# Kernel optimization log

Measured on AMD Instinct MI355X. Metric: run time of the kernel, lower is better.

The kernel has to match this reference:

```python
import math
import jax, jax.numpy as jnp
import numpy as np

E_EDGES = 65536
N_NODES = 8192
MUL = 32
LAT = 128
COND = 32
# uuu tensor-product instructions (l1, l2, l_out) generated by the selection-rule loop
INSTR = [(0,0,0),(1,1,0),(2,2,0),
         (0,1,1),(1,0,1),(1,1,1),(1,2,1),(2,1,1),(2,2,1),
         (0,2,2),(1,1,2),(1,2,2),(2,0,2),(2,1,2),(2,2,2)]

# ---- real Wigner-3j (invariant 3-tensor) via null space of equivariance constraints ----
def _su2_J(l):
    m = np.arange(-l, l + 1)
    Jz = np.diag(m).astype(complex)
    d = 2 * l + 1
    Jp = np.zeros((d, d), complex)
    Jp[np.arange(1, d), np.arange(0, d - 1)] = np.sqrt((l - m[:-1]) * (l + m[:-1] + 1))
    Jm = Jp.conj().T
    return (Jp + Jm) / 2, (Jp - Jm) / 2j, Jz

def _q(l):
    q = np.zeros((2 * l + 1, 2 * l + 1), complex)
    for m in range(-l, 0):
        q[l + m, l + abs(m)] = 1 / np.sqrt(2)
        q[l + m, l - abs(m)] = -1j / np.sqrt(2)
    q[l, l] = 1.0
    for m in range(1, l + 1):
        q[l + m, l + abs(m)] = (-1) ** m / np.sqrt(2)
        q[l + m, l - abs(m)] = 1j * (-1) ** m / np.sqrt(2)
    return q

def _gen(l):
    q = _q(l)
    return [np.real(q.conj().T @ (-1j * J) @ q) for J in _su2_J(l)]

def _w3j(l1, l2, l3):
    G1, G2, G3 = _gen(l1), _gen(l2), _gen(l3)
    d1, d2, d3 = 2 * l1 + 1, 2 * l2 + 1, 2 * l3 + 1
    rows = []
    for a in range(3):
        rows.append(np.kron(np.kron(G1[a], np.eye(d2)), np.eye(d3))
                    + np.kron(np.kron(np.eye(d1), G2[a]), np.eye(d3))
                    + np.kron(np.kron(np.eye(d1), np.eye(d2)), G3[a]))
    _, _, vt = np.linalg.svd(np.concatenate(rows, 0))
    c = vt[-1]
    c = c / np.linalg.norm(c)
    c = c * np.sign(c[np.argmax(np.abs(c))])
    return c.reshape(d1, d2, d3).astype(np.float32)

W3J = {}
for _k in INSTR:
    if _k not in W3J:
        W3J[_k] = jnp.asarray(_w3j(*_k))

def _split9(x):
    # (E, MUL, 9) -> per-l blocks (widths 1,3,5)
    return (x[:, :, 0:1], x[:, :, 1:4], x[:, :, 4:9])

def _so3_ln(blocks, gamma, eps=1e-6):
    out = []
    for b, x in enumerate(blocks):
        if x.shape[-1] == 1:  # scalars: centered layernorm over channels
            mu = jnp.mean(x, axis=1, keepdims=True)
            var = jnp.mean((x - mu) ** 2, axis=1, keepdims=True)
            x = (x - mu) * jax.lax.rsqrt(var + eps)
        else:  # l>0: RMS over (channel, m), no centering (equivariance)
            ms = jnp.mean(x ** 2, axis=(1, 2), keepdims=True)
            x = x * jax.lax.rsqrt(ms + eps)
        out.append(x * gamma[b][None, :, None])
    return out

def _forward(scalar_latent, equiv_latent, edge_conditioning, update_coeff,
             W_env, b_env0, gamma_env, Wg_env, bg_env, gamma_tp,
             W1_s, b1_s, W2_s, b2_s, Weq0, beq0, Weq1, Weq2, Wg_eq, bg_eq,
             edge_index, active_edges):
    E = scalar_latent.shape[0]
    edge_center = edge_index[0]
    # env_eq: per-l SO3 linear (channel mixing), bias on l=0
    xb = _split9(equiv_latent)
    env = [jnp.einsum('eum,vu->evm', xb[l], W_env[l]) for l in range(3)]
    env[0] = env[0] + b_env0[None, :, None]
    gate_in = jnp.concatenate([scalar_latent, edge_conditioning], axis=-1)  # (E,160)
    g_env = 1.0 + 0.1 * jnp.tanh(gate_in @ Wg_env + bg_env[0])
    env_edges = jnp.concatenate(env, axis=-1) * g_env[:, None, None]
    # scatter-sum edges -> nodes, SO3 layernorm, gather back per edge
    env_nodes = jax.ops.segment_sum(env_edges, edge_center, num_segments=N_NODES)
    env_nodes = jnp.concatenate(_so3_ln(_split9(env_nodes), gamma_env), axis=-1)
    local = env_nodes[edge_center]  # (E, MUL, 9)
    # selection-rule-sparse tensor product, uuu, component-normalized
    x1b = _split9(equiv_latent)
    x2b = _split9(local)
    tp_blocks = [math.sqrt(2 * lo + 1) * jnp.einsum('ijk,eui,euj->euk', W3J[(l1, l2, lo)], x1b[l1], x2b[l2])
                 for (l1, l2, lo) in INSTR]
    tp_blocks = _so3_ln(tp_blocks, gamma_tp)
    # scalar (l=0) slices -> (E, 3*MUL)
    tp_scalars = jnp.concatenate(tp_blocks[0:3], axis=-1).reshape(E, -1)
    scalar_in = jnp.concatenate([tp_scalars, edge_conditioning], axis=-1)
    new_scalar = jax.nn.silu(scalar_in @ W1_s.T + b1_s) @ W2_s.T + b2_s  # (E, LAT)
    # equiv_update: SO3 linear tp_out_irreps -> equiv_latent_irreps
    x0 = tp_scalars  # (E, 3*MUL)
    out0 = (x0 @ Weq0.T + beq0)[:, :, None]                      # (E, MUL, 1)
    out1 = jnp.einsum('eum,vu->evm', jnp.concatenate(tp_blocks[3:9], axis=1), Weq1)   # (E, MUL, 3)
    out2 = jnp.einsum('eum,vu->evm', jnp.concatenate(tp_blocks[9:15], axis=1), Weq2)  # (E, MUL, 5)
    new_equiv = jnp.concatenate([out0, out1, out2], axis=-1)
    g_eq = 1.0 + 0.1 * jnp.tanh(gate_in @ Wg_eq + bg_eq[0])
    new_equiv = new_equiv * g_eq[:, None, None]
    # residual stream with update coefficient + index_add over active_edges
    c = update_coeff[0]
    co = jax.lax.rsqrt(c * c + 1.0)
    cn = c * co
    s_out = (co * scalar_latent).at[active_edges].add(cn * new_scalar)
    e_out = (co * equiv_latent).at[active_edges].add(cn * new_equiv)
    return s_out, e_out

def setup_inputs() -> dict:
    key = jax.random.key(0)
    ks = jax.random.split(key, 16)
    f32 = jnp.float32
    return {
        'scalar_latent': jax.random.normal(ks[0], (E_EDGES, LAT), f32),
        'equiv_latent': jax.random.normal(ks[1], (E_EDGES, MUL, 9), f32),
        'edge_conditioning': jax.random.normal(ks[2], (E_EDGES, COND), f32),
        'update_coeff': jnp.ones((1,), f32),
        'W_env': jax.random.normal(ks[3], (3, MUL, MUL), f32) / math.sqrt(MUL),
        'b_env0': jnp.zeros((MUL,), f32),
        'gamma_env': jnp.ones((3, MUL), f32),
        'Wg_env': jax.random.normal(ks[4], (LAT + COND,), f32) / math.sqrt(LAT + COND),
        'bg_env': jnp.zeros((1,), f32),
        'gamma_tp': jnp.ones((15, MUL), f32),
        'W1_s': jax.random.normal(ks[5], (LAT, 3 * MUL + COND), f32) / math.sqrt(3 * MUL + COND),
        'b1_s': jnp.zeros((LAT,), f32),
        'W2_s': jax.random.normal(ks[6], (LAT, LAT), f32) / math.sqrt(LAT),
        'b2_s': jnp.zeros((LAT,), f32),
        'Weq0': jax.random.normal(ks[7], (MUL, 3 * MUL), f32) / math.sqrt(3 * MUL),
        'beq0': jnp.zeros((MUL,), f32),
        'Weq1': jax.random.normal(ks[8], (MUL, 6 * MUL), f32) / math.sqrt(6 * MUL),
        'Weq2': jax.random.normal(ks[9], (MUL, 6 * MUL), f32) / math.sqrt(6 * MUL),
        'Wg_eq': jax.random.normal(ks[10], (LAT + COND,), f32) / math.sqrt(LAT + COND),
        'bg_eq': jnp.zeros((1,), f32),
        'edge_index': jax.random.randint(ks[11], (2, E_EDGES), 0, N_NODES),
        'active_edges': jnp.arange(E_EDGES),
    }

def reference(scalar_latent, equiv_latent, edge_conditioning, update_coeff,
              W_env, b_env0, gamma_env, Wg_env, bg_env, gamma_tp,
              W1_s, b1_s, W2_s, b2_s, Weq0, beq0, Weq1, Weq2, Wg_eq, bg_eq,
              edge_index, active_edges):
    return _forward(scalar_latent, equiv_latent, edge_conditioning, update_coeff,
                    W_env, b_env0, gamma_env, Wg_env, bg_env, gamma_tp,
                    W1_s, b1_s, W2_s, b2_s, Weq0, beq0, Weq1, Weq2, Wg_eq, bg_eq,
                    edge_index, active_edges)
```

## Files before the change

kernel.cpp:

```cpp
#include <hip/hip_runtime.h>
#include <math.h>

#define E_EDGES 65536
#define N_NODES 8192

typedef _Float16 half_t;
typedef _Float16 h8 __attribute__((ext_vector_type(8)));
typedef float f4 __attribute__((ext_vector_type(4)));

#define SSC_P 136

#define C3f   0.57735026918962576f
#define C5f   0.44721359549995794f
#define C10f  0.31622776601683794f
#define C30f  0.18257418583505536f
#define C30x2 0.36514837167011072f
#define A235  0.23904572186687872f
#define B370  0.20701966780270626f
#define C70f  0.11952286093343936f
#define S3f   1.7320508075688772f
#define S5f   2.2360679774997896f
#define S5n  -2.2360679774997896f


__device__ double factd(int n) { double r = 1.0; for (int i = 2; i <= n; ++i) r *= i; return r; }

__device__ double w3j_m(int j1, int j2, int j3, int m1, int m2, int m3) {
  if (m1 + m2 + m3 != 0) return 0.0;
  if (abs(m1) > j1 || abs(m2) > j2 || abs(m3) > j3) return 0.0;
  double delta = sqrt(factd(j1 + j2 - j3) * factd(j1 - j2 + j3) * factd(-j1 + j2 + j3)
                      / factd(j1 + j2 + j3 + 1));
  double pref = sqrt(factd(j1 + m1) * factd(j1 - m1) * factd(j2 + m2) * factd(j2 - m2)
                     * factd(j3 + m3) * factd(j3 - m3));
  int klo = max(0, max(j2 - j3 - m1, j1 + m2 - j3));
  int khi = min(j1 + j2 - j3, min(j1 - m1, j2 + m2));
  double s = 0.0;
  for (int k = klo; k <= khi; ++k) {
    double d = factd(k) * factd(j1 + j2 - j3 - k) * factd(j1 - m1 - k) * factd(j2 + m2 - k)
             * factd(j3 - j2 + m1 + k) * factd(j3 - j1 - m2 + k);
    s += ((k & 1) ? -1.0 : 1.0) / d;
  }
  int e = j1 - j2 - m3;
  double sg = ((e % 2 + 2) % 2) ? -1.0 : 1.0;
  return sg * delta * pref * s;
}

__device__ void qent(int l, int mr, int col, double* re, double* im) {
  const double v = 0.7071067811865475244;
  *re = 0.0; *im = 0.0;
  int m = mr - l;
  if (m < 0) {
    if (col == l - m) *re = v;
    else if (col == l + m) *im = -v;
  } else if (m == 0) {
    if (col == l) *re = 1.0;
  } else {
    double s = (m & 1) ? -1.0 : 1.0;
    if (col == l + m) *re = s * v;
    else if (col == l - m) *im = s * v;
  }
}

__constant__ const int GB_L1[15] = {0,1,2,0,1,1,1,2,2,0,1,1,2,2,2};
__constant__ const int GB_L2[15] = {0,1,2,1,0,1,2,1,2,2,1,2,0,1,2};
__constant__ const int GB_LO[15] = {0,0,0,1,1,1,1,1,1,2,2,2,2,2,2};
__constant__ const int GB_WOFF[15] = {0,1,10,35,44,53,80,125,170,245,270,315,390,415,490};
__constant__ const double GB_FLIP[15] = {1,1,1,1,1,-1,1,1,1,1,1,1,1,-1,-1};

extern "C" __global__ __launch_bounds__(128)
void gen_w3j(float* __restrict__ w3j_out) {
  __shared__ double vsh[128];
  __shared__ double red[128];
  __shared__ int redi[128];
  const int b = blockIdx.x;
  const int t = threadIdx.x;
  const int l1 = GB_L1[b], l2 = GB_L2[b], l3 = GB_LO[b];
  const int d1 = 2 * l1 + 1, d2 = 2 * l2 + 1, d3 = 2 * l3 + 1;
  const int n = d1 * d2 * d3;
  double tre = 0.0, tim = 0.0;
  if (t < n) {
    int a = t / (d2 * d3), r = t - a * (d2 * d3), bb = r / d3, c = r - bb * d3;
    for (int mr1 = 0; mr1 < d1; ++mr1) {
      double q1r, q1i; qent(l1, mr1, a, &q1r, &q1i); q1i = -q1i;
      if (q1r == 0.0 && q1i == 0.0) continue;
      int m1 = mr1 - l1;
      for (int mr2 = 0; mr2 < d2; ++mr2) {
        double q2r, q2i; qent(l2, mr2, bb, &q2r, &q2i); q2i = -q2i;
        if (q2r == 0.0 && q2i == 0.0) continue;
        int m2 = mr2 - l2;
        int m3 = -(m1 + m2);
        if (m3 < -l3 || m3 > l3) continue;
        double q3r, q3i; qent(l3, m3 + l3, c, &q3r, &q3i); q3i = -q3i;
        if (q3r == 0.0 && q3i == 0.0) continue;
        double w = w3j_m(l1, l2, l3, m1, m2, m3);
        if (w == 0.0) continue;
        double ar = q1r * q2r - q1i * q2i, ai = q1r * q2i + q1i * q2r;
        double cr = ar * q3r - ai * q3i, ci = ar * q3i + ai * q3r;
        tre += cr * w; tim += ci * w;
      }
    }
  }
  red[t] = tre * tre; __syncthreads();
  for (int s = 64; s; s >>= 1) { if (t < s) red[t] += red[t + s]; __syncthreads(); }
  double nre = red[0]; __syncthreads();
  red[t] = tim * tim; __syncthreads();
  for (int s = 64; s; s >>= 1) { if (t < s) red[t] += red[t + s]; __syncthreads(); }
  double nim = red[0]; __syncthreads();
  double v = (nre >= nim) ? tre : tim;
  v *= 1.0 / sqrt(nre >= nim ? nre : nim);
  red[t] = fabs(v); __syncthreads();
  for (int s = 64; s; s >>= 1) { if (t < s) red[t] = fmax(red[t], red[t + s]); __syncthreads(); }
  double mx = red[0]; __syncthreads();
  redi[t] = (t < n && fabs(v) >= mx * (1.0 - 1e-6)) ? t : 1 << 20; __syncthreads();
  for (int s = 64; s; s >>= 1) { if (t < s) redi[t] = min(redi[t], redi[t + s]); __syncthreads(); }
  int win = redi[0];
  vsh[t] = v; __syncthreads();
  double sgn = (vsh[win] < 0.0) ? -1.0 : 1.0;
  const double norm3[3] = {1.0, 1.7320508075688772, 2.2360679774997896};
  if (t < n) w3j_out[GB_WOFF[b] + t] = (float)(v * sgn * GB_FLIP[b] * norm3[l3]);
}

extern "C" __global__ __launch_bounds__(256)
void prep_weights(const float* __restrict__ W1, const float* __restrict__ W2,
                  const float* __restrict__ Weq0, const float* __restrict__ Weq1,
                  const float* __restrict__ Weq2,
                  half_t* __restrict__ W1F, half_t* __restrict__ W2F,
                  half_t* __restrict__ Weq0F, half_t* __restrict__ Weq1F,
                  half_t* __restrict__ Weq2F) {
  int t = blockIdx.x * blockDim.x + threadIdx.x;
  int stride = gridDim.x * blockDim.x;
  for (int f = t; f < 16384; f += stride) {
    int i = f & 7, lane = (f >> 3) & 63, ks = (f >> 9) & 3, nt = f >> 11;
    int n = nt * 16 + (lane & 15);
    int k = ks * 32 + (lane >> 4) * 8 + i;
    W1F[f] = (half_t)W1[n * 128 + k];
    W2F[f] = (half_t)W2[n * 128 + k];
  }
  for (int f = t; f < 3072; f += stride) {
    int i = f & 7, lane = (f >> 3) & 63, rest = f >> 9;
    int ks = rest % 3, nt = rest / 3;
    int n = nt * 16 + (lane & 15);
    int k = ks * 32 + (lane >> 4) * 8 + i;
    Weq0F[f] = (half_t)Weq0[n * 96 + k];
  }
  for (int f = t; f < 6144; f += stride) {
    int i = f & 7, lane = (f >> 3) & 63, rest = f >> 9;
    int ks = rest % 6, nt = rest / 6;
    int n = nt * 16 + (lane & 15);
    int k = ks * 32 + (lane >> 4) * 8 + i;
    Weq1F[f] = (half_t)Weq1[n * 192 + k];
    Weq2F[f] = (half_t)Weq2[n * 192 + k];
  }
}

extern "C" __global__ __launch_bounds__(256)
void gate_count(const float* __restrict__ scalar, const float* __restrict__ cond,
                const float* __restrict__ Wg_env, const float* __restrict__ bg_env,
                const float* __restrict__ Wg_eq, const float* __restrict__ bg_eq,
                const int* __restrict__ edge_index,
                float* __restrict__ g_env, float* __restrict__ g_eq,
                int* __restrict__ counts) {
  const int t = threadIdx.x;
  const int e0 = blockIdx.x * 8;
  const int eg = t >> 5, lane = t & 31;
  size_t e = (size_t)(e0 + eg);
  float pa = 0.f, pb = 0.f;
  for (int i = lane; i < 160; i += 32) {
    float xi = (i < 128) ? scalar[e * 128 + i] : cond[e * 32 + (i - 128)];
    pa = fmaf(xi, Wg_env[i], pa);
    pb = fmaf(xi, Wg_eq[i], pb);
  }
  for (int off = 16; off; off >>= 1) { pa += __shfl_xor(pa, off); pb += __shfl_xor(pb, off); }
  if (lane == 0) {
    g_env[e] = 1.f + 0.1f * tanhf(pa + bg_env[0]);
    g_eq[e]  = 1.f + 0.1f * tanhf(pb + bg_eq[0]);
  }
  if (t < 8) atomicAdd(&counts[edge_index[e0 + t]], 1);
}

extern "C" __global__ __launch_bounds__(256)
void csr_scan(int* __restrict__ counts, int* __restrict__ offsets) {
  __shared__ int part[256];
  __shared__ int pre[257];
  const int t = threadIdx.x;
  const int base = t * 32;
  int s = 0;
  for (int i = 0; i < 32; ++i) s += counts[base + i];
  part[t] = s; __syncthreads();
  if (t == 0) { int a = 0; for (int i = 0; i < 256; ++i) { pre[i] = a; a += part[i]; } pre[256] = a; }
  __syncthreads();
  int run = pre[t];
  for (int i = 0; i < 32; ++i) {
    int c = counts[base + i];
    offsets[base + i] = run;
    counts[base + i] = run;
    run += c;
  }
  if (t == 0) offsets[N_NODES] = pre[256];
}

extern "C" __global__ __launch_bounds__(256)
void csr_fill(const int* __restrict__ edge_index, int* __restrict__ cursor,
              int* __restrict__ elist) {
  int e = blockIdx.x * 256 + threadIdx.x;
  if (e < E_EDGES) {
    int pos = atomicAdd(&cursor[edge_index[e]], 1);
    elist[pos] = e;
  }
}

extern "C" __global__ __launch_bounds__(128)
void env_build(const float* __restrict__ equiv, const float* __restrict__ g_env,
               const int* __restrict__ elist, const int* __restrict__ offsets,
               const float* __restrict__ W_env, const float* __restrict__ b_env0,
               const float* __restrict__ gamma_env, float* __restrict__ env_nodes) {
  __shared__ float xs[288];
  const int n = blockIdx.x, t = threadIdx.x;
  const int lo = offsets[n], hi = offsets[n + 1];
  float acc0 = 0.f, acc1 = 0.f, acc2 = 0.f, gsum = 0.f;
  for (int idx = lo; idx < hi; ++idx) {
    int e = elist[idx];
    float g = g_env[e];
    gsum += g;
    const float* row = equiv + (size_t)e * 288;
    acc0 = fmaf(g, row[t], acc0);
    acc1 = fmaf(g, row[t + 128], acc1);
    if (t < 32) acc2 = fmaf(g, row[t + 256], acc2);
  }
  xs[t] = acc0; xs[t + 128] = acc1;
  if (t < 32) xs[t + 256] = acc2;
  __syncthreads();
  float ev[9];
  if (t < 32) {
    const int v = t;
#pragma unroll
    for (int m = 0; m < 9; ++m) {
      int l = (m == 0) ? 0 : (m < 4 ? 1 : 2);
      const float4* Wr = (const float4*)(W_env + (size_t)(l * 32 + v) * 32);
      float s = 0.f;
#pragma unroll
      for (int u4 = 0; u4 < 8; ++u4) {
        float4 wv = Wr[u4];
        int ub = u4 * 4;
        s = fmaf(wv.x, xs[(ub + 0) * 9 + m], s);
        s = fmaf(wv.y, xs[(ub + 1) * 9 + m], s);
        s = fmaf(wv.z, xs[(ub + 2) * 9 + m], s);
        s = fmaf(wv.w, xs[(ub + 3) * 9 + m], s);
      }
      if (m == 0) s += b_env0[v] * gsum;
      ev[m] = s;
    }
    float s0 = ev[0], q0 = ev[0] * ev[0];
#pragma unroll
    for (int off = 16; off; off >>= 1) { s0 += __shfl_xor(s0, off); q0 += __shfl_xor(q0, off); }
    float mean0 = s0 * (1.f / 32.f);
    float var0 = q0 * (1.f / 32.f) - mean0 * mean0;
    float r0 = rsqrtf(var0 + 1e-6f);
    float q1 = ev[1] * ev[1] + ev[2] * ev[2] + ev[3] * ev[3];
#pragma unroll
    for (int off = 16; off; off >>= 1) q1 += __shfl_xor(q1, off);
    float r1 = rsqrtf(q1 * (1.f / 96.f) + 1e-6f);
    float q2 = ev[4]*ev[4] + ev[5]*ev[5] + ev[6]*ev[6] + ev[7]*ev[7] + ev[8]*ev[8];
#pragma unroll
    for (int off = 16; off; off >>= 1) q2 += __shfl_xor(q2, off);
    float r2 = rsqrtf(q2 * (1.f / 160.f) + 1e-6f);
    ev[0] = (ev[0] - mean0) * r0 * gamma_env[v];
    float g1 = r1 * gamma_env[32 + v], g2 = r2 * gamma_env[64 + v];
    ev[1] *= g1; ev[2] *= g1; ev[3] *= g1;
    ev[4] *= g2; ev[5] *= g2; ev[6] *= g2; ev[7] *= g2; ev[8] *= g2;
  }
  __syncthreads();
  if (t < 32) {
#pragma unroll
    for (int m = 0; m < 9; ++m) xs[t * 9 + m] = ev[m];
  }
  __syncthreads();
  float* outb = env_nodes + (size_t)n * 288;
  outb[t] = xs[t]; outb[t + 128] = xs[t + 128];
  if (t < 32) outb[t + 256] = xs[t + 256];
}

extern "C" __global__ __launch_bounds__(512, 4)
void edge_update(const float* __restrict__ scalar, const float* __restrict__ equiv,
                 const float* __restrict__ cond, const float* __restrict__ updc,
                 const float* __restrict__ env_nodes, const float* __restrict__ gamma_tp,
                 const half_t* __restrict__ W1F, const float* __restrict__ b1,
                 const half_t* __restrict__ W2F, const float* __restrict__ b2,
                 const half_t* __restrict__ Weq0F, const float* __restrict__ beq0,
                 const half_t* __restrict__ Weq1F, const half_t* __restrict__ Weq2F,
                 const float* __restrict__ g_eq,
                 const int* __restrict__ edge_index, const int* __restrict__ active_edges,
                 const float* __restrict__ w3j, float* __restrict__ out_s,
                 float* __restrict__ out_e) {
  __shared__ __align__(16) half_t stp[48 * 16 * 32];
  __shared__ __align__(16) half_t ssc[16 * SSC_P];
  __shared__ __align__(16) half_t shh[16 * SSC_P];
  __shared__ float sg[16];
  __shared__ int snode[16];
  __shared__ int sact[16];
  const int t = threadIdx.x;
  const int e0 = blockIdx.x * 16;
  const float cc = updc[0];
  const float co = rsqrtf(cc * cc + 1.f);
  const float cn = cc * co;

  if (t < 16) {
    snode[t] = edge_index[e0 + t];
    sact[t] = active_edges[e0 + t];
    sg[t] = g_eq[e0 + t];
  }
  {
    int e = t >> 5, j = t & 31;
    ssc[e * SSC_P + 96 + j] = (half_t)cond[(size_t)(e0 + e) * 32 + j];
  }
  __syncthreads();

  {
    const int eg = t >> 5, u = t & 31;
    const float* arow = equiv + (size_t)(e0 + eg) * 288 + u * 9;
    const float* brow = env_nodes + (size_t)snode[eg] * 288 + u * 9;
    float a0 = arow[0], b0 = brow[0];
    float A1[3] = {arow[1], arow[2], arow[3]};
    float A2[5] = {arow[4], arow[5], arow[6], arow[7], arow[8]};
    float B1[3] = {brow[1], brow[2], brow[3]};
    float B2[5] = {brow[4], brow[5], brow[6], brow[7], brow[8]};
    float o[51];
    o[0] = a0 * b0;
    o[1] = C3f * (A1[0]*B1[0] + A1[1]*B1[1] + A1[2]*B1[2]);
    o[2] = C5f * (A2[0]*B2[0] + A2[1]*B2[1] + A2[2]*B2[2] + A2[3]*B2[3] + A2[4]*B2[4]);
    o[3] = a0 * B1[0]; o[4] = a0 * B1[1]; o[5] = a0 * B1[2];
    o[6] = A1[0] * b0; o[7] = A1[1] * b0; o[8] = A1[2] * b0;
    o[9] = o[10] = o[11] = 0.f;
#pragma unroll
    for (int i = 0; i < 3; ++i)
#pragma unroll
      for (int j = 0; j < 3; ++j) {
        float p = A1[i] * B1[j];
#pragma unroll
        for (int k = 0; k < 3; ++k)
          o[9 + k] = fmaf(w3j[53 + (i * 3 + j) * 3 + k], p, o[9 + k]);
      }
    o[12] = S3f * (C10f*(A1[1]*B2[1] + A1[2]*B2[0]) - C30f*A1[0]*B2[2] - C10f*A1[0]*B2[4]);
    o[13] = S3f * (C10f*(A1[0]*B2[1] + A1[2]*B2[3]) + C30x2*A1[1]*B2[2]);
    o[14] = S3f * (C10f*(A1[0]*B2[0] + A1[1]*B2[3] + A1[2]*B2[4]) - C30f*A1[2]*B2[2]);
    o[15] = S3f * (C10f*(A2[1]*B1[1] + A2[0]*B1[2]) - C30f*A2[2]*B1[0] - C10f*A2[4]*B1[0]);
    o[16] = S3f * (C10f*(A2[1]*B1[0] + A2[3]*B1[2]) + C30x2*A2[2]*B1[1]);
    o[17] = S3f * (C10f*(A2[0]*B1[0] + A2[3]*B1[1] + A2[4]*B1[2]) - C30f*A2[2]*B1[2]);
    o[18] = o[19] = o[20] = 0.f;
#pragma unroll
    for (int i = 0; i < 5; ++i)
#pragma unroll
      for (int j = 0; j < 5; ++j) {
        float p = A2[i] * B2[j];
#pragma unroll
        for (int k = 0; k < 3; ++k)
          o[18 + k] = fmaf(w3j[170 + (i * 5 + j) * 3 + k], p, o[18 + k]);
      }
    o[21] = a0 * B2[0]; o[22] = a0 * B2[1]; o[23] = a0 * B2[2]; o[24] = a0 * B2[3]; o[25] = a0 * B2[4];
    o[26] = S5f * C10f * (A1[2]*B1[0] + A1[0]*B1[2]);
    o[27] = S5f * C10f * (A1[0]*B1[1] + A1[1]*B1[0]);
    o[28] = S5f * (C30x2*A1[1]*B1[1] - C30f*(A1[0]*B1[0] + A1[2]*B1[2]));
    o[29] = S5f * C10f * (A1[1]*B1[2] + A1[2]*B1[1]);
    o[30] = S5f * C10f * (A1[2]*B1[2] - A1[0]*B1[0]);
    o[31] = S5f * (C30f*(A1[2]*B2[3] - A1[0]*B2[1]) - C30x2*A1[1]*B2[4]);
    o[32] = S5f * (C30f*(A1[0]*B2[0] - A1[1]*B2[3] + A1[2]*B2[4]) + C10f*A1[2]*B2[2]);
    o[33] = S5f * C10f * (A1[0]*B2[3] - A1[2]*B2[1]);
    o[34] = S5f * (C30f*(A1[1]*B2[1] - A1[2]*B2[0] + A1[0]*B2[4]) - C10f*A1[0]*B2[2]);
    o[35] = S5f * (C30x2*A1[1]*B2[0] - C30f*(A1[2]*B2[1] + A1[0]*B2[3]));
    o[36] = A2[0] * b0; o[37] = A2[1] * b0; o[38] = A2[2] * b0; o[39] = A2[3] * b0; o[40] = A2[4] * b0;
    o[41] = S5n * (C30f*(A2[3]*B1[2] - A2[1]*B1[0]) - C30x2*A2[4]*B1[1]);
    o[42] = S5n * (C30f*(A2[0]*B1[0] - A2[3]*B1[1] + A2[4]*B1[2]) + C10f*A2[2]*B1[2]);
    o[43] = S5n * C10f * (A2[3]*B1[0] - A2[1]*B1[2]);
    o[44] = S5n * (C30f*(A2[1]*B1[1] - A2[0]*B1[2] + A2[4]*B1[0]) - C10f*A2[2]*B1[0]);
    o[45] = S5n * (C30x2*A2[0]*B1[1] - C30f*(A2[1]*B1[2] + A2[3]*B1[0]));
    o[46] = S5n * (A235*(A2[0]*B2[2] + A2[2]*B2[0]) - B370*(A2[1]*B2[3] + A2[3]*B2[1]));
    o[47] = S5n * (-B370*(A2[0]*B2[3] + A2[3]*B2[0]) - C70f*(A2[1]*B2[2] + A2[2]*B2[1]) + B370*(A2[1]*B2[4] + A2[4]*B2[1]));
    o[48] = S5n * (A235*(A2[0]*B2[0] - A2[2]*B2[2] + A2[4]*B2[4]) - C70f*(A2[1]*B2[1] + A2[3]*B2[3]));
    o[49] = S5n * (-B370*(A2[0]*B2[1] + A2[1]*B2[0]) - C70f*(A2[3]*B2[2] + A2[2]*B2[3]) - B370*(A2[3]*B2[4] + A2[4]*B2[3]));
    o[50] = S5n * (B370*(A2[1]*B2[1] - A2[3]*B2[3]) + A235*(A2[2]*B2[4] + A2[4]*B2[2]));

#pragma unroll
    for (int b = 0; b < 3; ++b) {
      float x = o[b];
      float s = x, q = x * x;
#pragma unroll
      for (int off = 16; off; off >>= 1) { s += __shfl_xor(s, off); q += __shfl_xor(q, off); }
      float mean = s * (1.f / 32.f);
      float var = q * (1.f / 32.f) - mean * mean;
      ssc[eg * SSC_P + u * 3 + b] = (half_t)((x - mean) * rsqrtf(var + 1e-6f) * gamma_tp[b * 32 + u]);
    }
    const int offs[12] = {3, 6, 9, 12, 15, 18, 21, 26, 31, 36, 41, 46};
    const int d3s[12]  = {3, 3, 3, 3, 3, 3, 5, 5, 5, 5, 5, 5};
    const int uswz = u ^ ((eg & 3) << 3);
#pragma unroll
    for (int bb = 0; bb < 12; ++bb) {
      float q = 0.f;
#pragma unroll
      for (int k = 0; k < d3s[bb]; ++k) { float x = o[offs[bb] + k]; q += x * x; }
#pragma unroll
      for (int off = 16; off; off >>= 1) q += __shfl_xor(q, off);
      float scale = rsqrtf(q / (32.f * d3s[bb]) + 1e-6f) * gamma_tp[(bb + 3) * 32 + u];
#pragma unroll
      for (int k = 0; k < d3s[bb]; ++k)
        stp[((offs[bb] + k - 3) * 16 + eg) * 32 + uswz] = (half_t)(o[offs[bb] + k] * scale);
    }
  }
  __syncthreads();

  const int l = t & 63, wave = t >> 6;
  const int g = l >> 4, c = l & 15;
  f4 mlp2acc;

  {
    const int nt = wave;
    float bn = b1[nt * 16 + c];
    f4 acc = {bn, bn, bn, bn};
#pragma unroll
    for (int ks = 0; ks < 4; ++ks) {
      h8 a = *(const h8*)&ssc[c * SSC_P + ks * 32 + g * 8];
      h8 b = *(const h8*)&W1F[(((nt * 4 + ks) * 64) + l) * 8];
      acc = __builtin_amdgcn_mfma_f32_16x16x32_f16(a, b, acc, 0, 0, 0);
    }
#pragma unroll
    for (int i = 0; i < 4; ++i) {
      float x = acc[i];
      shh[(4 * g + i) * SSC_P + nt * 16 + c] = (half_t)(x / (1.f + expf(-x)));
    }
  }
  __syncthreads();

  {
    const int nt = wave;
    float bn = b2[nt * 16 + c];
    f4 acc = {bn, bn, bn, bn};
#pragma unroll
    for (int ks = 0; ks < 4; ++ks) {
      h8 a = *(const h8*)&shh[c * SSC_P + ks * 32 + g * 8];
      h8 b = *(const h8*)&W2F[(((nt * 4 + ks) * 64) + l) * 8];
      acc = __builtin_amdgcn_mfma_f32_16x16x32_f16(a, b, acc, 0, 0, 0);
    }
    mlp2acc = acc;
  }

  f4 accT[3];
  int nTiles = 0;
  for (int T = wave; T < 18; T += 8, ++nTiles) {
    f4 acc;
    if (T < 2) {
      const int nt = T;
      float bv = beq0[nt * 16 + c];
      acc = (f4){bv, bv, bv, bv};
#pragma unroll
      for (int ks = 0; ks < 3; ++ks) {
        h8 a = *(const h8*)&ssc[c * SSC_P + ks * 32 + g * 8];
        h8 b = *(const h8*)&Weq0F[(((nt * 3 + ks) * 64) + l) * 8];
        acc = __builtin_amdgcn_mfma_f32_16x16x32_f16(a, b, acc, 0, 0, 0);
      }
    } else if (T < 8) {
      const int idx = T - 2, Mt = idx >> 1, nt = idx & 1;
      const int row = Mt * 16 + c;
      const int e = row / 3, m = row - e * 3;
      const int gx = (g ^ (e & 3)) * 8;
      acc = (f4){0.f, 0.f, 0.f, 0.f};
#pragma unroll
      for (int ks = 0; ks < 6; ++ks) {
        int kk = ks * 3 + m;
        h8 a = *(const h8*)&stp[(kk * 16 + e) * 32 + gx];
        h8 b = *(const h8*)&Weq1F[(((nt * 6 + ks) * 64) + l) * 8];
        acc = __builtin_amdgcn_mfma_f32_16x16x32_f16(a, b, acc, 0, 0, 0);
      }
    } else {
      const int idx = T - 8, Mt = idx >> 1, nt = idx & 1;
      const int row = Mt * 16 + c;
      const int e = row / 5, m = row - e * 5;
      const int gx = (g ^ (e & 3)) * 8;
      acc = (f4){0.f, 0.f, 0.f, 0.f};
#pragma unroll
      for (int ks = 0; ks < 6; ++ks) {
        int kk = 18 + ks * 5 + m;
        h8 a = *(const h8*)&stp[(kk * 16 + e) * 32 + gx];
        h8 b = *(const h8*)&Weq2F[(((nt * 6 + ks) * 64) + l) * 8];
        acc = __builtin_amdgcn_mfma_f32_16x16x32_f16(a, b, acc, 0, 0, 0);
      }
    }
    accT[nTiles] = acc;
  }
  __syncthreads();

  {
    float* tmp  = reinterpret_cast<float*>(&stp[0]);
    float* sout = tmp + 4608;
    int slot = 0;
    for (int T = wave; T < 18; T += 8, ++slot) {
      f4 acc = accT[slot];
      int Mt, nt, type;
      if (T < 2)      { type = 0; Mt = 0; nt = T; }
      else if (T < 8) { type = 1; Mt = (T - 2) >> 1; nt = (T - 2) & 1; }
      else            { type = 2; Mt = (T - 8) >> 1; nt = (T - 8) & 1; }
      const int v = nt * 16 + c;
#pragma unroll
      for (int i = 0; i < 4; ++i) {
        int row = Mt * 16 + 4 * g + i;
        int e, off;
        if (type == 0)      { e = row; off = 0; }
        else if (type == 1) { e = row / 3; off = 1 + (row - e * 3); }
        else                { e = row / 5; off = 4 + (row - e * 5); }
        tmp[e * 288 + v * 9 + off] = cn * sg[e] * acc[i];
      }
    }
    {
      const int nt = wave;
#pragma unroll
      for (int i = 0; i < 4; ++i)
        sout[(4 * g + i) * 128 + nt * 16 + c] = cn * mlp2acc[i];
    }
  }
  __syncthreads();

  {
    const float* tmp  = reinterpret_cast<const float*>(&stp[0]);
    const float* sout = tmp + 4608;
    const float4* tmp4 = (const float4*)tmp;
    for (int i = t; i < 16 * 72; i += 512) {
      int e = i / 72, q = i - e * 72;
      size_t r = (size_t)sact[e];
      const float4 ev = *(const float4*)&equiv[r * 288 + q * 4];
      float4 tv = tmp4[i];
      float4 ov;
      ov.x = co * ev.x + tv.x; ov.y = co * ev.y + tv.y;
      ov.z = co * ev.z + tv.z; ov.w = co * ev.w + tv.w;
      *(float4*)&out_e[r * 288 + q * 4] = ov;
    }
    for (int i = t; i < 16 * 128; i += 512) {
      int e = i >> 7, n = i & 127;
      size_t r = (size_t)sact[e];
      out_s[r * 128 + n] = co * scalar[r * 128 + n] + sout[i];
    }
  }
}

extern "C" void kernel_launch(void* const* d_in, const int* in_sizes, int n_in,
                              void* d_out, int out_size, void* d_ws, size_t ws_size,
                              hipStream_t stream) {
  const float* scalar     = (const float*)d_in[0];
  const float* equiv      = (const float*)d_in[1];
  const float* cond       = (const float*)d_in[2];
  const float* updc       = (const float*)d_in[3];
  const float* W_env      = (const float*)d_in[4];
  const float* b_env0     = (const float*)d_in[5];
  const float* gamma_env  = (const float*)d_in[6];
  const float* Wg_env     = (const float*)d_in[7];
  const float* bg_env     = (const float*)d_in[8];
  const float* gamma_tp   = (const float*)d_in[9];
  const float* W1         = (const float*)d_in[10];
  const float* b1         = (const float*)d_in[11];
  const float* W2         = (const float*)d_in[12];
  const float* b2         = (const float*)d_in[13];
  const float* Weq0       = (const float*)d_in[14];
  const float* beq0       = (const float*)d_in[15];
  const float* Weq1       = (const float*)d_in[16];
  const float* Weq2       = (const float*)d_in[17];
  const float* Wg_eq      = (const float*)d_in[18];
  const float* bg_eq      = (const float*)d_in[19];
  const int* edge_index   = (const int*)d_in[20];
  const int* active_edges = (const int*)d_in[21];

  float* out_s = (float*)d_out;
  float* out_e = out_s + (size_t)E_EDGES * 128;

  float* ws    = (float*)d_ws;
  float* env   = ws;
  float* w3jt  = env + (size_t)N_NODES * 288;
  float* diag  = w3jt + 640;
  half_t* W1F   = (half_t*)(diag + 16);
  half_t* W2F   = W1F + 16384;
  half_t* Weq0F = W2F + 16384;
  half_t* Weq1F = Weq0F + 3072;
  half_t* Weq2F = Weq1F + 6144;
  int* counts  = (int*)(Weq2F + 6144);
  int* offsets = counts + N_NODES;
  float* g_eq  = (float*)(offsets + N_NODES + 1);
  float* g_env = out_s + ((size_t)E_EDGES * (128 + 288) - 131072);
  int* elist   = (int*)(g_env + 65536);

  hipMemsetAsync(counts, 0, N_NODES * sizeof(int), stream);
  gen_w3j<<<15, 128, 0, stream>>>(w3jt);
  prep_weights<<<48, 256, 0, stream>>>(W1, W2, Weq0, Weq1, Weq2,
                                       W1F, W2F, Weq0F, Weq1F, Weq2F);
  gate_count<<<E_EDGES / 8, 256, 0, stream>>>(scalar, cond, Wg_env, bg_env, Wg_eq, bg_eq,
                                              edge_index, g_env, g_eq, counts);
  csr_scan<<<1, 256, 0, stream>>>(counts, offsets);
  csr_fill<<<E_EDGES / 256, 256, 0, stream>>>(edge_index, counts, elist);
  env_build<<<N_NODES, 128, 0, stream>>>(equiv, g_env, elist, offsets,
                                         W_env, b_env0, gamma_env, env);
  edge_update<<<E_EDGES / 16, 512, 0, stream>>>(scalar, equiv, cond, updc, env, gamma_tp,
                                                W1F, b1, W2F, b2, Weq0F, beq0, Weq1F, Weq2F,
                                                g_eq, edge_index, active_edges,
                                                w3jt, out_s, out_e);
}
```

Baseline: 241.6 us.

## Merge gate computation into CSR fill and split env_build gather across two groups

Moves the gate computation out of the counting pass and into the fill pass. The count pass becomes a plain atomic histogram, and the separate fill kernel goes away. env_build now runs 256 threads per node: two groups each accumulate alternating incoming edges, with two edges per iteration for more loads in flight, and the partial sums are combined through shared memory. This targets latency in the per-node gather, at the cost of an extra shared reduction and sync. Edge order within each node's list still depends on atomics.

New measurement: 261.6 us. +8.3%, slower.

```diff
diff --git a/kernel.cpp b/kernel.cpp
--- a/kernel.cpp
+++ b/kernel.cpp
@@ -154,28 +154,9 @@
 }
 
 extern "C" __global__ __launch_bounds__(256)
-void gate_count(const float* __restrict__ scalar, const float* __restrict__ cond,
-                const float* __restrict__ Wg_env, const float* __restrict__ bg_env,
-                const float* __restrict__ Wg_eq, const float* __restrict__ bg_eq,
-                const int* __restrict__ edge_index,
-                float* __restrict__ g_env, float* __restrict__ g_eq,
-                int* __restrict__ counts) {
-  const int t = threadIdx.x;
-  const int e0 = blockIdx.x * 8;
-  const int eg = t >> 5, lane = t & 31;
-  size_t e = (size_t)(e0 + eg);
-  float pa = 0.f, pb = 0.f;
-  for (int i = lane; i < 160; i += 32) {
-    float xi = (i < 128) ? scalar[e * 128 + i] : cond[e * 32 + (i - 128)];
-    pa = fmaf(xi, Wg_env[i], pa);
-    pb = fmaf(xi, Wg_eq[i], pb);
-  }
-  for (int off = 16; off; off >>= 1) { pa += __shfl_xor(pa, off); pb += __shfl_xor(pb, off); }
-  if (lane == 0) {
-    g_env[e] = 1.f + 0.1f * tanhf(pa + bg_env[0]);
-    g_eq[e]  = 1.f + 0.1f * tanhf(pb + bg_eq[0]);
-  }
-  if (t < 8) atomicAdd(&counts[edge_index[e0 + t]], 1);
+void csr_count(const int* __restrict__ edge_index, int* __restrict__ counts) {
+  int e = blockIdx.x * 256 + threadIdx.x;
+  if (e < E_EDGES) atomicAdd(&counts[edge_index[e]], 1);
 }
 
 extern "C" __global__ __launch_bounds__(256)
@@ -200,36 +181,79 @@
 }
 
 extern "C" __global__ __launch_bounds__(256)
-void csr_fill(const int* __restrict__ edge_index, int* __restrict__ cursor,
-              int* __restrict__ elist) {
-  int e = blockIdx.x * 256 + threadIdx.x;
-  if (e < E_EDGES) {
-    int pos = atomicAdd(&cursor[edge_index[e]], 1);
-    elist[pos] = e;
-  }
-}
-
-extern "C" __global__ __launch_bounds__(128)
+void gate_fill(const float* __restrict__ scalar, const float* __restrict__ cond,
+               const float* __restrict__ Wg_env, const float* __restrict__ bg_env,
+               const float* __restrict__ Wg_eq, const float* __restrict__ bg_eq,
+               const int* __restrict__ edge_index,
+               float* __restrict__ g_env, float* __restrict__ g_eq,
+               int* __restrict__ cursor, int* __restrict__ elist) {
+  const int t = threadIdx.x;
+  const int e0 = blockIdx.x * 8;
+  const int eg = t >> 5, lane = t & 31;
+  size_t e = (size_t)(e0 + eg);
+  float pa = 0.f, pb = 0.f;
+  for (int i = lane; i < 160; i += 32) {
+    float xi = (i < 128) ? scalar[e * 128 + i] : cond[e * 32 + (i - 128)];
+    pa = fmaf(xi, Wg_env[i], pa);
+    pb = fmaf(xi, Wg_eq[i], pb);
+  }
+  for (int off = 16; off; off >>= 1) { pa += __shfl_xor(pa, off); pb += __shfl_xor(pb, off); }
+  if (lane == 0) {
+    g_env[e] = 1.f + 0.1f * tanhf(pa + bg_env[0]);
+    g_eq[e]  = 1.f + 0.1f * tanhf(pb + bg_eq[0]);
+  }
+  if (t < 8) {
+    int ge = e0 + t;
+    int pos = atomicAdd(&cursor[edge_index[ge]], 1);
+    elist[pos] = ge;
+  }
+}
+
+extern "C" __global__ __launch_bounds__(256)
 void env_build(const float* __restrict__ equiv, const float* __restrict__ g_env,
                const int* __restrict__ elist, const int* __restrict__ offsets,
                const float* __restrict__ W_env, const float* __restrict__ b_env0,
                const float* __restrict__ gamma_env, float* __restrict__ env_nodes) {
   __shared__ float xs[288];
+  __shared__ float xs2[288];
+  __shared__ float gsums[2];
   const int n = blockIdx.x, t = threadIdx.x;
+  const int grp = t >> 7, tt = t & 127;
   const int lo = offsets[n], hi = offsets[n + 1];
   float acc0 = 0.f, acc1 = 0.f, acc2 = 0.f, gsum = 0.f;
-  for (int idx = lo; idx < hi; ++idx) {
+  int idx = lo + grp;
+  for (; idx + 2 < hi; idx += 4) {
+    int ea = elist[idx], eb = elist[idx + 2];
+    float ga = g_env[ea], gb = g_env[eb];
+    gsum += ga + gb;
+    const float* ra = equiv + (size_t)ea * 288;
+    const float* rb = equiv + (size_t)eb * 288;
+    float a0 = ra[tt], b0 = rb[tt];
+    float a1 = ra[tt + 128], b1v = rb[tt + 128];
+    acc0 = fmaf(ga, a0, acc0); acc0 = fmaf(gb, b0, acc0);
+    acc1 = fmaf(ga, a1, acc1); acc1 = fmaf(gb, b1v, acc1);
+    if (tt < 32) {
+      acc2 = fmaf(ga, ra[tt + 256], acc2);
+      acc2 = fmaf(gb, rb[tt + 256], acc2);
+    }
+  }
+  for (; idx < hi; idx += 2) {
     int e = elist[idx];
     float g = g_env[e];
     gsum += g;
     const float* row = equiv + (size_t)e * 288;
-    acc0 = fmaf(g, row[t], acc0);
-    acc1 = fmaf(g, row[t + 128], acc1);
-    if (t < 32) acc2 = fmaf(g, row[t + 256], acc2);
-  }
-  xs[t] = acc0; xs[t + 128] = acc1;
-  if (t < 32) xs[t + 256] = acc2;
-  __syncthreads();
+    acc0 = fmaf(g, row[tt], acc0);
+    acc1 = fmaf(g, row[tt + 128], acc1);
+    if (tt < 32) acc2 = fmaf(g, row[tt + 256], acc2);
+  }
+  float* dst = grp ? xs2 : xs;
+  dst[tt] = acc0; dst[tt + 128] = acc1;
+  if (tt < 32) dst[tt + 256] = acc2;
+  if (tt == 0) gsums[grp] = gsum;
+  __syncthreads();
+  for (int i = t; i < 288; i += 256) xs[i] += xs2[i];
+  __syncthreads();
+  float gsumT = gsums[0] + gsums[1];
   float ev[9];
   if (t < 32) {
     const int v = t;
@@ -247,7 +271,7 @@
         s = fmaf(wv.z, xs[(ub + 2) * 9 + m], s);
         s = fmaf(wv.w, xs[(ub + 3) * 9 + m], s);
       }
-      if (m == 0) s += b_env0[v] * gsum;
+      if (m == 0) s += b_env0[v] * gsumT;
       ev[m] = s;
     }
     float s0 = ev[0], q0 = ev[0] * ev[0];
@@ -276,8 +300,7 @@
   }
   __syncthreads();
   float* outb = env_nodes + (size_t)n * 288;
-  outb[t] = xs[t]; outb[t + 128] = xs[t + 128];
-  if (t < 32) outb[t + 256] = xs[t + 256];
+  for (int i = t; i < 288; i += 256) outb[i] = xs[i];
 }
 
 extern "C" __global__ __launch_bounds__(512, 4)
@@ -587,11 +610,11 @@
   gen_w3j<<<15, 128, 0, stream>>>(w3jt);
   prep_weights<<<48, 256, 0, stream>>>(W1, W2, Weq0, Weq1, Weq2,
                                        W1F, W2F, Weq0F, Weq1F, Weq2F);
-  gate_count<<<E_EDGES / 8, 256, 0, stream>>>(scalar, cond, Wg_env, bg_env, Wg_eq, bg_eq,
-                                              edge_index, g_env, g_eq, counts);
+  csr_count<<<E_EDGES / 256, 256, 0, stream>>>(edge_index, counts);
   csr_scan<<<1, 256, 0, stream>>>(counts, offsets);
-  csr_fill<<<E_EDGES / 256, 256, 0, stream>>>(edge_index, counts, elist);
-  env_build<<<N_NODES, 128, 0, stream>>>(equiv, g_env, elist, offsets,
+  gate_fill<<<E_EDGES / 8, 256, 0, stream>>>(scalar, cond, Wg_env, bg_env, Wg_eq, bg_eq,
+                                             edge_index, g_env, g_eq, counts, elist);
+  env_build<<<N_NODES, 256, 0, stream>>>(equiv, g_env, elist, offsets,
                                          W_env, b_env0, gamma_env, env);
   edge_update<<<E_EDGES / 16, 512, 0, stream>>>(scalar, equiv, cond, updc, env, gamma_tp,
                                                 W1F, b1, W2F, b2, Weq0F, beq0, Weq1F, Weq2F,
```
